# Optimization experiments

Hardware: AMD Instinct MI355X
Metric: run time of the kernel (lower is better)

The kernel has to match this reference:

```python
import jax, jax.numpy as jnp
import numpy as np

T = 256        # number of save/step points
BATCH = 2048   # batched trajectories
DATA = 32      # state dim (data_size)
WIDTH = 128    # MLP width
DELAYS = (1.0, 2.0)  # constant delays tau_j (all >> dt so lookups are in the past)


def setup_inputs() -> dict:
    key = jax.random.key(0)
    ks = jax.random.split(key, 5)
    ts = jnp.linspace(0.0, 10.0, T, dtype=jnp.float32)
    y0 = jax.random.normal(ks[0], (BATCH, DATA), dtype=jnp.float32)
    in_size = (len(DELAYS) + 1) * DATA  # (nb_delays + 1) * data_size

    def lin(k, o, i):
        kw, kb = jax.random.split(k)
        lim = 1.0 / np.sqrt(i)
        W = jax.random.uniform(kw, (o, i), jnp.float32, -lim, lim)
        b = jax.random.uniform(kb, (o,), jnp.float32, -lim, lim)
        return W, b

    W0, b0 = lin(ks[1], WIDTH, in_size)   # in -> width
    W1, b1 = lin(ks[2], WIDTH, WIDTH)     # hidden
    W2, b2 = lin(ks[3], WIDTH, WIDTH)     # hidden
    W3, b3 = lin(ks[4], DATA, WIDTH)      # width -> out (no activation)
    return dict(ts=ts, y0=y0, W0=W0, b0=b0, W1=W1, b1=b1, W2=W2, b2=b2, W3=W3, b3=b3)


def _mlp(x, W0, b0, W1, b1, W2, b2, W3, b3):
    # eqx.nn.MLP(depth=3, activation=relu): 4 linears, relu after hidden layers
    h = jax.nn.relu(x @ W0.T + b0)
    h = jax.nn.relu(h @ W1.T + b1)
    h = jax.nn.relu(h @ W2.T + b2)
    return h @ W3.T + b3


def _solve(ts, y0, params):
    t0 = ts[0]
    dt0 = ts[1] - ts[0]

    def lookup(buf, t):
        # linear interpolation of stored history on the uniform grid;
        # t <= t0 clips to index 0 where buf[0] == y0 (constant initial history)
        s = jnp.clip((t - t0) / dt0, 0.0, T - 1.0)
        i0 = jnp.floor(s).astype(jnp.int32)
        i1 = jnp.minimum(i0 + 1, T - 1)
        w = s - i0.astype(s.dtype)
        return (1.0 - w) * buf[i0] + w * buf[i1]

    def f(t, y, buf):
        hist = [lookup(buf, t - tau) for tau in DELAYS]
        return _mlp(jnp.concatenate([y] + hist, axis=-1), *params)

    buf0 = jnp.zeros((T, BATCH, DATA), y0.dtype).at[0].set(y0)

    def step(carry, inp):
        y, buf = carry
        i, t, t_next = inp
        dt = t_next - t
        # Bosh3 / Bogacki-Shampine stages
        k1 = f(t, y, buf)
        k2 = f(t + 0.5 * dt, y + 0.5 * dt * k1, buf)
        k3 = f(t + 0.75 * dt, y + 0.75 * dt * k2, buf)
        y_next = y + dt * (2.0 / 9.0 * k1 + 1.0 / 3.0 * k2 + 4.0 / 9.0 * k3)
        buf = buf.at[i + 1].set(y_next)
        return (y_next, buf), y_next

    xs = (jnp.arange(T - 1), ts[:-1], ts[1:])
    (_, _), ys_tail = jax.lax.scan(step, (y0, buf0), xs)
    return jnp.concatenate([y0[None], ys_tail], axis=0)  # [T, BATCH, DATA]


def reference(ts, y0, W0, b0, W1, b1, W2, b2, W3, b3):
    ys = _solve(ts, y0, (W0, b0, W1, b1, W2, b2, W3, b3))
    return ys, jnp.int32(T - 1)  # (solution.ys, num_steps)
```

## Files before the change

kernel.cpp:

```cpp
#include <hip/hip_runtime.h>

#define TT 256
#define BATCH 2048
#define DATA 32
#define WSLOTS 52

typedef __bf16 bf16x8 __attribute__((ext_vector_type(8)));
typedef float f32x4 __attribute__((ext_vector_type(4)));

#define MFMA(A, B, C) __builtin_amdgcn_mfma_f32_16x16x32_bf16((A), (B), (C), 0, 0, 0)

union bfp2 { uint2 u; __bf16 b[4]; };
union bfp4 { uint4 q; bf16x8 v; __bf16 b[8]; };

__device__ __forceinline__ bf16x8 ldw8(const float* __restrict__ p) {
    float4 a = *(const float4*)p;
    float4 b = *(const float4*)(p + 4);
    bf16x8 r;
    r[0] = (__bf16)a.x; r[1] = (__bf16)a.y; r[2] = (__bf16)a.z; r[3] = (__bf16)a.w;
    r[4] = (__bf16)b.x; r[5] = (__bf16)b.y; r[6] = (__bf16)b.z; r[7] = (__bf16)b.w;
    return r;
}

__device__ __forceinline__ bf16x8 ldx(const char* base, int row, int kbyte) {
    return *(const bf16x8*)(base + row * 256 + (kbyte ^ ((row & 7) << 4)));
}

#define HID1(WF, KC, SRC, DST, BI)                                                    \
    {                                                                                 \
        bf16x8 xf[4];                                                                 \
        _Pragma("unroll") for (int kc = 0; kc < (KC); ++kc)                           \
            xf[kc] = ldx(SRC, m, kc * 64 + g * 16);                                   \
        f32x4 a0 = BI;                                                                \
        _Pragma("unroll") for (int kc = 0; kc < (KC); ++kc)                           \
            a0 = MFMA(WF[kc], xf[kc], a0);                                            \
        bfp2 p0;                                                                      \
        _Pragma("unroll") for (int j = 0; j < 4; ++j)                                 \
            p0.b[j] = (__bf16)fmaxf(a0[j], 0.0f);                                     \
        *(uint2*)((DST) + m * 256 + ((tbB2 + g * 8) ^ sw)) = p0.u;                    \
    }

#define PRELERP(TQT, XDST)                                                            \
    {                                                                                 \
        const int   dl  = wv - 2;                                                     \
        const float tau = dl ? 2.0f : 1.0f;                                           \
        float s = ((TQT) - tau - t0v) * ivd0;                                         \
        s = fminf(fmaxf(s, 0.0f), 255.0f);                                            \
        const int   i0 = (int)s;                                                      \
        const int   i1 = min(i0 + 1, TT - 1);                                         \
        const float w  = s - (float)i0;                                               \
        bfp4 pa, pb, pr;                                                              \
        pa.v = *(const bf16x8*)(hists + (i0 % WSLOTS) * 1280 + m * 80 + g * 16);      \
        pb.v = *(const bf16x8*)(hists + (i1 % WSLOTS) * 1280 + m * 80 + g * 16);      \
        _Pragma("unroll") for (int e = 0; e < 8; ++e) {                               \
            const float va = (float)pa.b[e];                                          \
            pr.b[e] = (__bf16)fmaf(w, (float)pb.b[e] - va, va);                       \
        }                                                                             \
        *(bf16x8*)((XDST) + dl * 1280 + m * 80 + g * 16) = pr.v;                      \
    }

#define DO_STAGE(USEK, CST, KP, KD, XSRC, XDST, TQT)                                  \
    {                                                                                 \
                                 \
        bfp4 xf0;                                                                     \
        _Pragma("unroll") for (int e = 0; e < 8; ++e)                                 \
            xf0.b[e] = (__bf16)((USEK) ? fmaf((CST) * dt, KP[e], y[e]) : y[e]);       \
        bf16x8 xl1 = *(const bf16x8*)((XSRC) + m * 80 + g * 16);                      \
        bf16x8 xl2 = *(const bf16x8*)((XSRC) + 1280 + m * 80 + g * 16);               \
        f32x4 a0 = bias0;                                                             \
        a0 = MFMA(W0f[0], xf0.v, a0);                                                 \
        a0 = MFMA(W0f[1], xl1, a0);                                                   \
        a0 = MFMA(W0f[2], xl2, a0);                                                   \
        bfp2 p0;                                                                      \
        _Pragma("unroll") for (int j = 0; j < 4; ++j)                                 \
            p0.b[j] = (__bf16)fmaxf(a0[j], 0.0f);                                     \
        *(uint2*)(hA + m * 256 + ((tbB2 + g * 8) ^ sw)) = p0.u;                       \
        __syncthreads();                                                              \
        HID1(W1f, 4, hA, hB, bias1)                                                   \
        __syncthreads();                                                              \
        HID1(W2f, 4, hB, hA, bias2)                                                   \
        __syncthreads();                                                              \
        if (wv < 2) {                      \
            bf16x8 xf[4];                                                             \
            _Pragma("unroll") for (int kc = 0; kc < 4; ++kc)                          \
                xf[kc] = ldx(hA, m, kc * 64 + g * 16);                                \
            f32x4 a = bias3;                                                          \
            _Pragma("unroll") for (int kc = 0; kc < 4; ++kc)                          \
                a = MFMA(W3f[kc], xf[kc], a);                                         \
            *(f32x4*)(kbuf + m * 128 + (((wv * 4 + g) ^ (m & 7)) << 4)) = a;          \
        } else if (wv < 4) {                                                          \
            PRELERP(TQT, XDST)                                                        \
        }                                                                             \
        __syncthreads();                                                              \
        {                           \
            f32x4 q0 = *(const f32x4*)(kbuf + m * 128 + (((2 * g) ^ (m & 7)) << 4));  \
            f32x4 q1 = *(const f32x4*)(kbuf + m * 128 + (((2 * g + 1) ^ (m & 7)) << 4)); \
            _Pragma("unroll") for (int j = 0; j < 4; ++j) {                           \
                KD[j] = q0[j]; KD[4 + j] = q1[j];                                     \
            }                                                                         \
        }                                                                             \
    }

__global__ __launch_bounds__(512, 1) void dde_8w(
    const float* __restrict__ ts, const float* __restrict__ y0,
    const float* __restrict__ W0, const float* __restrict__ b0,
    const float* __restrict__ W1, const float* __restrict__ b1,
    const float* __restrict__ W2, const float* __restrict__ b2,
    const float* __restrict__ W3, const float* __restrict__ b3,
    float* __restrict__ out)
{
    __shared__ __align__(16) char hists[WSLOTS * 1280];
    __shared__ __align__(16) char xb0[2 * 1280];
    __shared__ __align__(16) char xb1[2 * 1280];
    __shared__ __align__(16) char xb2[2 * 1280];
    __shared__ __align__(16) char hA[16 * 256];
    __shared__ __align__(16) char hB[16 * 256];
    __shared__ __align__(16) char kbuf[16 * 128];
    __shared__ float tsb[TT];

    const int tid  = threadIdx.x;
    const int lane = tid & 63;
    const int wv   = tid >> 6;
    const int m    = lane & 15;
    const int g    = lane >> 4;
    const int tbB2 = wv * 32;
    const int sw   = (m & 7) << 4;
    const int R0   = blockIdx.x * 16;

    for (int idx = tid; idx < WSLOTS * 320; idx += 512) ((unsigned*)hists)[idx] = 0u;
    if (tid < TT) tsb[tid] = ts[tid];

    bf16x8 W0f[3], W1f[4], W2f[4], W3f[4];
    {
        const int rw = wv * 16 + m;
        #pragma unroll
        for (int kc = 0; kc < 3; ++kc) W0f[kc] = ldw8(W0 + rw * 96 + kc * 32 + g * 8);
        #pragma unroll
        for (int kc = 0; kc < 4; ++kc) W1f[kc] = ldw8(W1 + rw * 128 + kc * 32 + g * 8);
        #pragma unroll
        for (int kc = 0; kc < 4; ++kc) W2f[kc] = ldw8(W2 + rw * 128 + kc * 32 + g * 8);
        const int rw3 = (wv & 1) * 16 + m;
        #pragma unroll
        for (int kc = 0; kc < 4; ++kc) W3f[kc] = ldw8(W3 + rw3 * 128 + kc * 32 + g * 8);
    }
    f32x4 bias0, bias1, bias2, bias3;
    bias0 = *(const f32x4*)(b0 + wv * 16 + g * 4);
    bias1 = *(const f32x4*)(b1 + wv * 16 + g * 4);
    bias2 = *(const f32x4*)(b2 + wv * 16 + g * 4);
    bias3 = *(const f32x4*)(b3 + (wv & 1) * 16 + g * 4);

    __syncthreads();

    float y[8], k1[8], k2[8], k3[8];
    {
        float4 v0 = *(const float4*)(y0 + (R0 + m) * DATA + g * 8);
        float4 v1 = *(const float4*)(y0 + (R0 + m) * DATA + g * 8 + 4);
        y[0] = v0.x; y[1] = v0.y; y[2] = v0.z; y[3] = v0.w;
        y[4] = v1.x; y[5] = v1.y; y[6] = v1.z; y[7] = v1.w;
        #pragma unroll
        for (int e = 0; e < 8; ++e) { k1[e] = 0.0f; k2[e] = 0.0f; k3[e] = 0.0f; }
        if (wv == 0) {
            bfp4 p;
            #pragma unroll
            for (int e = 0; e < 8; ++e) p.b[e] = (__bf16)y[e];
            *(bf16x8*)(hists + m * 80 + g * 16) = p.v;
            *(float4*)(out + (R0 + m) * DATA + g * 8) = v0;
            *(float4*)(out + (R0 + m) * DATA + g * 8 + 4) = v1;
        }
    }
    if (blockIdx.x == 0 && tid == 0)
        out[(size_t)TT * BATCH * DATA] = 255.0f;
    __syncthreads();

    const float t0v  = tsb[0];
    const float ivd0 = 1.0f / (tsb[1] - tsb[0]);

    if (wv >= 2 && wv < 4) {
        const float dt0 = tsb[1] - tsb[0];
        PRELERP(t0v, xb0)
        PRELERP(fmaf(0.5f, dt0, t0v), xb1)
        PRELERP(fmaf(0.75f, dt0, t0v), xb2)
    }
    __syncthreads();

    #pragma unroll 1
    for (int i = 0; i < TT - 1; ++i) {
        const float t   = tsb[i];
        const float tn  = tsb[i + 1];
        const float dt  = tn - t;
        const float tnn = tsb[min(i + 2, TT - 1)];
        const float dtn = tnn - tn;

        DO_STAGE(0, 0.0f,  k1, k1, xb0, xb2, fmaf(0.75f, dt, t))
        DO_STAGE(1, 0.5f,  k1, k2, xb1, xb0, tn)
        DO_STAGE(2, 0.75f, k2, k3, xb2, xb1, fmaf(0.5f, dtn, tn))

        {
            #pragma unroll
            for (int e = 0; e < 8; ++e) {
                const float ks = (2.0f / 9.0f) * k1[e] + (1.0f / 3.0f) * k2[e]
                               + (4.0f / 9.0f) * k3[e];
                y[e] = fmaf(dt, ks, y[e]);
            }
            if (wv == 0) {
                bfp4 p;
                #pragma unroll
                for (int e = 0; e < 8; ++e) p.b[e] = (__bf16)y[e];
                *(bf16x8*)(hists + ((i + 1) % WSLOTS) * 1280 + m * 80 + g * 16) = p.v;
                float4 o0, o1;
                o0.x = y[0]; o0.y = y[1]; o0.z = y[2]; o0.w = y[3];
                o1.x = y[4]; o1.y = y[5]; o1.z = y[6]; o1.w = y[7];
                float* op = out + (size_t)(i + 1) * BATCH * DATA + (R0 + m) * DATA + g * 8;
                *(float4*)op = o0;
                *(float4*)(op + 4) = o1;
            }
        }
    }
}

extern "C" void kernel_launch(void* const* d_in, const int* in_sizes, int n_in,
                              void* d_out, int out_size, void* d_ws, size_t ws_size,
                              hipStream_t stream) {
    const float* ts = (const float*)d_in[0];
    const float* y0 = (const float*)d_in[1];
    const float* W0 = (const float*)d_in[2];
    const float* b0 = (const float*)d_in[3];
    const float* W1 = (const float*)d_in[4];
    const float* b1 = (const float*)d_in[5];
    const float* W2 = (const float*)d_in[6];
    const float* b2 = (const float*)d_in[7];
    const float* W3 = (const float*)d_in[8];
    const float* b3 = (const float*)d_in[9];

    dde_8w<<<dim3(BATCH / 16), dim3(512), 0, stream>>>(
        ts, y0, W0, b0, W1, b1, W2, b2, W3, b3, (float*)d_out);
}
```

Before: 717.6 us.

## Replicate output layer in every wave to drop a barrier and shared k buffer

```diff
diff --git a/kernel.cpp b/kernel.cpp
--- a/kernel.cpp
+++ b/kernel.cpp
@@ -10,8 +10,9 @@
 
 #define MFMA(A, B, C) __builtin_amdgcn_mfma_f32_16x16x32_bf16((A), (B), (C), 0, 0, 0)
 
-union bfp2 { uint2 u; __bf16 b[4]; };
-union bfp4 { uint4 q; bf16x8 v; __bf16 b[8]; };
+union bfp2 { unsigned u; __bf16 b[2]; };
+union bfq  { uint2 u; __bf16 b[4]; };
+union bfx8 { uint4 q; bf16x8 v; __bf16 b[8]; unsigned w[4]; };
 
 __device__ __forceinline__ bf16x8 ldw8(const float* __restrict__ p) {
     float4 a = *(const float4*)p;
@@ -31,77 +32,112 @@
         bf16x8 xf[4];                                                                 \
         _Pragma("unroll") for (int kc = 0; kc < (KC); ++kc)                           \
             xf[kc] = ldx(SRC, m, kc * 64 + g * 16);                                   \
-        f32x4 a0 = BI;                                                                \
+        f32x4 ac = BI;                                                                \
         _Pragma("unroll") for (int kc = 0; kc < (KC); ++kc)                           \
-            a0 = MFMA(WF[kc], xf[kc], a0);                                            \
-        bfp2 p0;                                                                      \
+            ac = MFMA(WF[kc], xf[kc], ac);                                            \
+        bfq p0;                                                                       \
         _Pragma("unroll") for (int j = 0; j < 4; ++j)                                 \
-            p0.b[j] = (__bf16)fmaxf(a0[j], 0.0f);                                     \
+            p0.b[j] = (__bf16)fmaxf(ac[j], 0.0f);                                     \
         *(uint2*)((DST) + m * 256 + ((tbB2 + g * 8) ^ sw)) = p0.u;                    \
     }
 
-#define PRELERP(TQT, XDST)                                                            \
+#define LERP2(TQT, O1, O2)                                                            \
     {                                                                                 \
-        const int   dl  = wv - 2;                                                     \
-        const float tau = dl ? 2.0f : 1.0f;                                           \
-        float s = ((TQT) - tau - t0v) * ivd0;                                         \
-        s = fminf(fmaxf(s, 0.0f), 255.0f);                                            \
-        const int   i0 = (int)s;                                                      \
-        const int   i1 = min(i0 + 1, TT - 1);                                         \
-        const float w  = s - (float)i0;                                               \
-        bfp4 pa, pb, pr;                                                              \
-        pa.v = *(const bf16x8*)(hists + (i0 % WSLOTS) * 1280 + m * 80 + g * 16);      \
-        pb.v = *(const bf16x8*)(hists + (i1 % WSLOTS) * 1280 + m * 80 + g * 16);      \
-        _Pragma("unroll") for (int e = 0; e < 8; ++e) {                               \
-            const float va = (float)pa.b[e];                                          \
-            pr.b[e] = (__bf16)fmaf(w, (float)pb.b[e] - va, va);                       \
-        }                                                                             \
-        *(bf16x8*)((XDST) + dl * 1280 + m * 80 + g * 16) = pr.v;                      \
-    }
-
-#define DO_STAGE(USEK, CST, KP, KD, XSRC, XDST, TQT)                                  \
+        _Pragma("unroll") for (int dl = 0; dl < 2; ++dl) {                            \
+            const float tau = dl ? 2.0f : 1.0f;                                       \
+            float s = ((TQT) - tau - t0v) * ivd0;                                     \
+            s = fminf(fmaxf(s, 0.0f), 255.0f);                                        \
+            const int   i0 = (int)s;                                                  \
+            const int   i1 = min(i0 + 1, TT - 1);                                     \
+            const float w  = s - (float)i0;                                           \
+            bfx8 pa, pb, pr;                                                          \
+            pa.v = *(const bf16x8*)(hists + (i0 % WSLOTS) * 1280 + m * 80 + g * 16);  \
+            pb.v = *(const bf16x8*)(hists + (i1 % WSLOTS) * 1280 + m * 80 + g * 16);  \
+            _Pragma("unroll") for (int e = 0; e < 8; ++e) {                           \
+                const float va = (float)pa.b[e];                                      \
+                pr.b[e] = (__bf16)fmaf(w, (float)pb.b[e] - va, va);                   \
+            }                                                                         \
+            if (dl == 0) O1 = pr.v; else O2 = pr.v;                                   \
+        }                                                                             \
+    }
+
+#define DO_STAGE(USEK, CST, KP, KD, XI1, XI2, XO1, XO2, TQN, FIN, I)                  \
     {                                                                                 \
-                                 \
-        bfp4 xf0;                                                                     \
-        _Pragma("unroll") for (int e = 0; e < 8; ++e)                                 \
-            xf0.b[e] = (__bf16)((USEK) ? fmaf((CST) * dt, KP[e], y[e]) : y[e]);       \
-        bf16x8 xl1 = *(const bf16x8*)((XSRC) + m * 80 + g * 16);                      \
-        bf16x8 xl2 = *(const bf16x8*)((XSRC) + 1280 + m * 80 + g * 16);               \
-        f32x4 a0 = bias0;                                                             \
-        a0 = MFMA(W0f[0], xf0.v, a0);                                                 \
-        a0 = MFMA(W0f[1], xl1, a0);                                                   \
-        a0 = MFMA(W0f[2], xl2, a0);                                                   \
-        bfp2 p0;                                                                      \
-        _Pragma("unroll") for (int j = 0; j < 4; ++j)                                 \
-            p0.b[j] = (__bf16)fmaxf(a0[j], 0.0f);                                     \
-        *(uint2*)(hA + m * 256 + ((tbB2 + g * 8) ^ sw)) = p0.u;                       \
+                      \
+        float yst[2][4];                                                              \
+        _Pragma("unroll") for (int t2 = 0; t2 < 2; ++t2)                              \
+            _Pragma("unroll") for (int j = 0; j < 4; ++j)                             \
+                yst[t2][j] = (USEK) ? fmaf((CST) * dt, KP[t2][j], y[t2][j])           \
+                                    : y[t2][j];                                       \
+        unsigned pk2[2][2];                                                           \
+        _Pragma("unroll") for (int t2 = 0; t2 < 2; ++t2)                              \
+            _Pragma("unroll") for (int s2 = 0; s2 < 2; ++s2) {                        \
+                bfp2 pp;                                                              \
+                pp.b[0] = (__bf16)yst[t2][2 * s2];                                    \
+                pp.b[1] = (__bf16)yst[t2][2 * s2 + 1];                                \
+                pk2[t2][s2] = pp.u;                                                   \
+            }                                                                         \
+        bfx8 xf0;                                                                     \
+        _Pragma("unroll") for (int s2 = 0; s2 < 2; ++s2) {                            \
+            int aa = __builtin_amdgcn_ds_bpermute(pa0, (int)pk2[0][s2]);              \
+            int bb = __builtin_amdgcn_ds_bpermute(pa0, (int)pk2[1][s2]);              \
+            int cc = __builtin_amdgcn_ds_bpermute(pa1, (int)pk2[0][s2]);              \
+            int dd = __builtin_amdgcn_ds_bpermute(pa1, (int)pk2[1][s2]);              \
+            xf0.w[s2]     = tsel ? (unsigned)bb : (unsigned)aa;                       \
+            xf0.w[2 + s2] = tsel ? (unsigned)dd : (unsigned)cc;                       \
+        }                                                                             \
+        {                                                                             \
+            f32x4 a0c = bias0;                                                        \
+            a0c = MFMA(W0f[1], XI1, a0c);         \
+            a0c = MFMA(W0f[2], XI2, a0c);                                             \
+            a0c = MFMA(W0f[0], xf0.v, a0c);                                           \
+            bfq p0;                                                                   \
+            _Pragma("unroll") for (int j = 0; j < 4; ++j)                             \
+                p0.b[j] = (__bf16)fmaxf(a0c[j], 0.0f);                                \
+            *(uint2*)(hA + m * 256 + ((tbB2 + g * 8) ^ sw)) = p0.u;                   \
+        }                                                                             \
         __syncthreads();                                                              \
         HID1(W1f, 4, hA, hB, bias1)                                                   \
         __syncthreads();                                                              \
-        HID1(W2f, 4, hB, hA, bias2)                                                   \
+        HID1(W2f, 4, hB, hC, bias2)                                                   \
         __syncthreads();                                                              \
-        if (wv < 2) {                      \
-            bf16x8 xf[4];                                                             \
+        {        \
+            LERP2(TQN, XO1, XO2)                                                      \
+            bf16x8 hx[4];                                                             \
             _Pragma("unroll") for (int kc = 0; kc < 4; ++kc)                          \
-                xf[kc] = ldx(hA, m, kc * 64 + g * 16);                                \
-            f32x4 a = bias3;                                                          \
-            _Pragma("unroll") for (int kc = 0; kc < 4; ++kc)                          \
-                a = MFMA(W3f[kc], xf[kc], a);                                         \
-            *(f32x4*)(kbuf + m * 128 + (((wv * 4 + g) ^ (m & 7)) << 4)) = a;          \
-        } else if (wv < 4) {                                                          \
-            PRELERP(TQT, XDST)                                                        \
-        }                                                                             \
-        __syncthreads();                                                              \
-        {                           \
-            f32x4 q0 = *(const f32x4*)(kbuf + m * 128 + (((2 * g) ^ (m & 7)) << 4));  \
-            f32x4 q1 = *(const f32x4*)(kbuf + m * 128 + (((2 * g + 1) ^ (m & 7)) << 4)); \
-            _Pragma("unroll") for (int j = 0; j < 4; ++j) {                           \
-                KD[j] = q0[j]; KD[4 + j] = q1[j];                                     \
-            }                                                                         \
-        }                                                                             \
-    }
-
-__global__ __launch_bounds__(512, 1) void dde_8w(
+                hx[kc] = ldx(hC, m, kc * 64 + g * 16);                                \
+            _Pragma("unroll") for (int t2 = 0; t2 < 2; ++t2) {                        \
+                f32x4 a3 = bias3D[t2];                                                \
+                _Pragma("unroll") for (int kc = 0; kc < 4; ++kc)                      \
+                    a3 = MFMA(W3f[t2][kc], hx[kc], a3);                               \
+                KD[t2] = a3;                                                          \
+            }                                                                         \
+            if (FIN) {                 \
+                _Pragma("unroll") for (int t2 = 0; t2 < 2; ++t2)                      \
+                    _Pragma("unroll") for (int j = 0; j < 4; ++j) {                   \
+                        const float ks = (2.0f / 9.0f) * k1[t2][j]                    \
+                                       + (1.0f / 3.0f) * k2[t2][j]                    \
+                                       + (4.0f / 9.0f) * KD[t2][j];                   \
+                        y[t2][j] = fmaf(dt, ks, y[t2][j]);                            \
+                    }                                                                 \
+                if (wv == 0) {                                                        \
+                    _Pragma("unroll") for (int t2 = 0; t2 < 2; ++t2) {                \
+                        bfq p; float4 v;                                              \
+                        p.b[0] = (__bf16)y[t2][0]; p.b[1] = (__bf16)y[t2][1];         \
+                        p.b[2] = (__bf16)y[t2][2]; p.b[3] = (__bf16)y[t2][3];         \
+                        v.x = y[t2][0]; v.y = y[t2][1];                               \
+                        v.z = y[t2][2]; v.w = y[t2][3];                               \
+                        *(uint2*)(hists + (((I) + 1) % WSLOTS) * 1280 + m * 80        \
+                                  + t2 * 32 + g * 8) = p.u;                           \
+                        *(float4*)(out + (size_t)((I) + 1) * BATCH * DATA             \
+                                   + (R0 + m) * DATA + t2 * 16 + g * 4) = v;          \
+                    }                                                                 \
+                }                                                                     \
+            }                                                                         \
+        }                                                                             \
+    }
+
+__global__ __launch_bounds__(512, 1) void dde_p(
     const float* __restrict__ ts, const float* __restrict__ y0,
     const float* __restrict__ W0, const float* __restrict__ b0,
     const float* __restrict__ W1, const float* __restrict__ b1,
@@ -110,12 +146,9 @@
     float* __restrict__ out)
 {
     __shared__ __align__(16) char hists[WSLOTS * 1280];
-    __shared__ __align__(16) char xb0[2 * 1280];
-    __shared__ __align__(16) char xb1[2 * 1280];
-    __shared__ __align__(16) char xb2[2 * 1280];
     __shared__ __align__(16) char hA[16 * 256];
     __shared__ __align__(16) char hB[16 * 256];
-    __shared__ __align__(16) char kbuf[16 * 128];
+    __shared__ __align__(16) char hC[16 * 256];
     __shared__ float tsb[TT];
 
     const int tid  = threadIdx.x;
@@ -126,11 +159,14 @@
     const int tbB2 = wv * 32;
     const int sw   = (m & 7) << 4;
     const int R0   = blockIdx.x * 16;
+    const int pa0  = (m + ((g & 1) << 5)) << 2;
+    const int pa1  = pa0 + 64;
+    const int tsel = g >> 1;
 
     for (int idx = tid; idx < WSLOTS * 320; idx += 512) ((unsigned*)hists)[idx] = 0u;
     if (tid < TT) tsb[tid] = ts[tid];
 
-    bf16x8 W0f[3], W1f[4], W2f[4], W3f[4];
+    bf16x8 W0f[3], W1f[4], W2f[4], W3f[2][4];
     {
         const int rw = wv * 16 + m;
         #pragma unroll
@@ -139,33 +175,34 @@
         for (int kc = 0; kc < 4; ++kc) W1f[kc] = ldw8(W1 + rw * 128 + kc * 32 + g * 8);
         #pragma unroll
         for (int kc = 0; kc < 4; ++kc) W2f[kc] = ldw8(W2 + rw * 128 + kc * 32 + g * 8);
-        const int rw3 = (wv & 1) * 16 + m;
-        #pragma unroll
-        for (int kc = 0; kc < 4; ++kc) W3f[kc] = ldw8(W3 + rw3 * 128 + kc * 32 + g * 8);
-    }
-    f32x4 bias0, bias1, bias2, bias3;
+        #pragma unroll
+        for (int t2 = 0; t2 < 2; ++t2)
+            #pragma unroll
+            for (int kc = 0; kc < 4; ++kc)
+                W3f[t2][kc] = ldw8(W3 + (t2 * 16 + m) * 128 + kc * 32 + g * 8);
+    }
+    f32x4 bias0, bias1, bias2, bias3D[2];
     bias0 = *(const f32x4*)(b0 + wv * 16 + g * 4);
     bias1 = *(const f32x4*)(b1 + wv * 16 + g * 4);
     bias2 = *(const f32x4*)(b2 + wv * 16 + g * 4);
-    bias3 = *(const f32x4*)(b3 + (wv & 1) * 16 + g * 4);
+    #pragma unroll
+    for (int t2 = 0; t2 < 2; ++t2)
+        bias3D[t2] = *(const f32x4*)(b3 + t2 * 16 + g * 4);
 
     __syncthreads();
 
-    float y[8], k1[8], k2[8], k3[8];
-    {
-        float4 v0 = *(const float4*)(y0 + (R0 + m) * DATA + g * 8);
-        float4 v1 = *(const float4*)(y0 + (R0 + m) * DATA + g * 8 + 4);
-        y[0] = v0.x; y[1] = v0.y; y[2] = v0.z; y[3] = v0.w;
-        y[4] = v1.x; y[5] = v1.y; y[6] = v1.z; y[7] = v1.w;
-        #pragma unroll
-        for (int e = 0; e < 8; ++e) { k1[e] = 0.0f; k2[e] = 0.0f; k3[e] = 0.0f; }
+    f32x4 y[2], k1[2], k2[2], k3[2];
+    #pragma unroll
+    for (int t2 = 0; t2 < 2; ++t2) {
+        float4 vv = *(const float4*)(y0 + (R0 + m) * DATA + t2 * 16 + g * 4);
+        y[t2][0] = vv.x; y[t2][1] = vv.y; y[t2][2] = vv.z; y[t2][3] = vv.w;
+        k1[t2] = f32x4{0.f, 0.f, 0.f, 0.f}; k2[t2] = k1[t2]; k3[t2] = k1[t2];
         if (wv == 0) {
-            bfp4 p;
-            #pragma unroll
-            for (int e = 0; e < 8; ++e) p.b[e] = (__bf16)y[e];
-            *(bf16x8*)(hists + m * 80 + g * 16) = p.v;
-            *(float4*)(out + (R0 + m) * DATA + g * 8) = v0;
-            *(float4*)(out + (R0 + m) * DATA + g * 8 + 4) = v1;
+            bfq p;
+            p.b[0] = (__bf16)vv.x; p.b[1] = (__bf16)vv.y;
+            p.b[2] = (__bf16)vv.z; p.b[3] = (__bf16)vv.w;
+            *(uint2*)(hists + m * 80 + t2 * 32 + g * 8) = p.u;
+            *(float4*)(out + (R0 + m) * DATA + t2 * 16 + g * 4) = vv;
         }
     }
     if (blockIdx.x == 0 && tid == 0)
@@ -175,46 +212,19 @@
     const float t0v  = tsb[0];
     const float ivd0 = 1.0f / (tsb[1] - tsb[0]);
 
-    if (wv >= 2 && wv < 4) {
-        const float dt0 = tsb[1] - tsb[0];
-        PRELERP(t0v, xb0)
-        PRELERP(fmaf(0.5f, dt0, t0v), xb1)
-        PRELERP(fmaf(0.75f, dt0, t0v), xb2)
-    }
-    __syncthreads();
+    bf16x8 xlA1, xlA2, xlB1, xlB2, xlC1, xlC2;
+    LERP2(t0v, xlA1, xlA2)
 
     #pragma unroll 1
     for (int i = 0; i < TT - 1; ++i) {
-        const float t   = tsb[i];
-        const float tn  = tsb[i + 1];
-        const float dt  = tn - t;
-        const float tnn = tsb[min(i + 2, TT - 1)];
-        const float dtn = tnn - tn;
-
-        DO_STAGE(0, 0.0f,  k1, k1, xb0, xb2, fmaf(0.75f, dt, t))
-        DO_STAGE(1, 0.5f,  k1, k2, xb1, xb0, tn)
-        DO_STAGE(2, 0.75f, k2, k3, xb2, xb1, fmaf(0.5f, dtn, tn))
-
-        {
-            #pragma unroll
-            for (int e = 0; e < 8; ++e) {
-                const float ks = (2.0f / 9.0f) * k1[e] + (1.0f / 3.0f) * k2[e]
-                               + (4.0f / 9.0f) * k3[e];
-                y[e] = fmaf(dt, ks, y[e]);
-            }
-            if (wv == 0) {
-                bfp4 p;
-                #pragma unroll
-                for (int e = 0; e < 8; ++e) p.b[e] = (__bf16)y[e];
-                *(bf16x8*)(hists + ((i + 1) % WSLOTS) * 1280 + m * 80 + g * 16) = p.v;
-                float4 o0, o1;
-                o0.x = y[0]; o0.y = y[1]; o0.z = y[2]; o0.w = y[3];
-                o1.x = y[4]; o1.y = y[5]; o1.z = y[6]; o1.w = y[7];
-                float* op = out + (size_t)(i + 1) * BATCH * DATA + (R0 + m) * DATA + g * 8;
-                *(float4*)op = o0;
-                *(float4*)(op + 4) = o1;
-            }
-        }
+        const float t  = tsb[i];
+        const float tn = tsb[i + 1];
+        const float dt = tn - t;
+
+        DO_STAGE(0, 0.0f,  k1, k1, xlA1, xlA2, xlB1, xlB2, fmaf(0.5f, dt, t), 0, i)
+        DO_STAGE(1, 0.5f,  k1, k2, xlB1, xlB2, xlC1, xlC2, fmaf(0.75f, dt, t), 0, i)
+        DO_STAGE(2, 0.75f, k2, k3, xlC1, xlC2, xlA1, xlA2, tn, 1, i)
+
     }
 }
 
@@ -232,6 +242,6 @@
     const float* W3 = (const float*)d_in[8];
     const float* b3 = (const float*)d_in[9];
 
-    dde_8w<<<dim3(BATCH / 16), dim3(512), 0, stream>>>(
+    dde_p<<<dim3(BATCH / 16), dim3(512), 0, stream>>>(
         ts, y0, W0, b0, W1, b1, W2, b2, W3, b3, (float*)d_out);
 }
```

Result: slower. 933.1 us (+30.0%).

## Fold output layer into first layer via precomputed W0y·W3 product

Applied to the files above, without the earlier changes.

```diff
diff --git a/kernel.cpp b/kernel.cpp
--- a/kernel.cpp
+++ b/kernel.cpp
@@ -26,82 +26,93 @@
     return *(const bf16x8*)(base + row * 256 + (kbyte ^ ((row & 7) << 4)));
 }
 
-#define HID1(WF, KC, SRC, DST, BI)                                                    \
+#define LERP2(TQT, O1, O2)                                                            \
+    {                                                                                 \
+        _Pragma("unroll") for (int dl = 0; dl < 2; ++dl) {                            \
+            const float tau = dl ? 2.0f : 1.0f;                                       \
+            float s = ((TQT) - tau - t0v) * ivd0;                                     \
+            s = fminf(fmaxf(s, 0.0f), 255.0f);                                        \
+            const int   i0 = (int)s;                                                  \
+            const int   i1 = min(i0 + 1, TT - 1);                                     \
+            const float w  = s - (float)i0;                                           \
+            bfp4 pa, pb, pr;                                                          \
+            pa.v = *(const bf16x8*)(hists + (i0 % WSLOTS) * 1280 + m * 80 + g * 16);  \
+            pb.v = *(const bf16x8*)(hists + (i1 % WSLOTS) * 1280 + m * 80 + g * 16);  \
+            _Pragma("unroll") for (int e = 0; e < 8; ++e) {                           \
+                const float va = (float)pa.b[e];                                      \
+                pr.b[e] = (__bf16)fmaf(w, (float)pb.b[e] - va, va);                   \
+            }                                                                         \
+            if (dl == 0) O1 = pr.v; else O2 = pr.v;                                   \
+        }                                                                             \
+    }
+
+#define SEGB()                                                                        \
     {                                                                                 \
         bf16x8 xf[4];                                                                 \
-        _Pragma("unroll") for (int kc = 0; kc < (KC); ++kc)                           \
-            xf[kc] = ldx(SRC, m, kc * 64 + g * 16);                                   \
-        f32x4 a0 = BI;                                                                \
-        _Pragma("unroll") for (int kc = 0; kc < (KC); ++kc)                           \
-            a0 = MFMA(WF[kc], xf[kc], a0);                                            \
+        _Pragma("unroll") for (int kc = 0; kc < 4; ++kc)                              \
+            xf[kc] = ldx(hA, m, kc * 64 + g * 16);                                    \
+        f32x4 a0 = b1D, cc = {0.f, 0.f, 0.f, 0.f};                                    \
+        __builtin_amdgcn_s_setprio(1);                                                \
+        a0 = MFMA(W1f[0], xf[0], a0); cc = MFMA(W1f[2], xf[2], cc);                   \
+        a0 = MFMA(W1f[1], xf[1], a0); cc = MFMA(W1f[3], xf[3], cc);                   \
+        __builtin_amdgcn_s_setprio(0);                                                \
         bfp2 p0;                                                                      \
         _Pragma("unroll") for (int j = 0; j < 4; ++j)                                 \
-            p0.b[j] = (__bf16)fmaxf(a0[j], 0.0f);                                     \
-        *(uint2*)((DST) + m * 256 + ((tbB2 + g * 8) ^ sw)) = p0.u;                    \
-    }
-
-#define PRELERP(TQT, XDST)                                                            \
+            p0.b[j] = (__bf16)fmaxf(a0[j] + cc[j], 0.0f);                             \
+        *(uint2*)(hB + m * 256 + ((tbB2 + g * 8) ^ sw)) = p0.u;                       \
+    }
+
+#define SEGC(COEF, FIRST, STOREH2, DSTBUF)                                            \
     {                                                                                 \
-        const int   dl  = wv - 2;                                                     \
-        const float tau = dl ? 2.0f : 1.0f;                                           \
-        float s = ((TQT) - tau - t0v) * ivd0;                                         \
-        s = fminf(fmaxf(s, 0.0f), 255.0f);                                            \
-        const int   i0 = (int)s;                                                      \
-        const int   i1 = min(i0 + 1, TT - 1);                                         \
-        const float w  = s - (float)i0;                                               \
-        bfp4 pa, pb, pr;                                                              \
-        pa.v = *(const bf16x8*)(hists + (i0 % WSLOTS) * 1280 + m * 80 + g * 16);      \
-        pb.v = *(const bf16x8*)(hists + (i1 % WSLOTS) * 1280 + m * 80 + g * 16);      \
-        _Pragma("unroll") for (int e = 0; e < 8; ++e) {                               \
-            const float va = (float)pa.b[e];                                          \
-            pr.b[e] = (__bf16)fmaf(w, (float)pb.b[e] - va, va);                       \
-        }                                                                             \
-        *(bf16x8*)((XDST) + dl * 1280 + m * 80 + g * 16) = pr.v;                      \
-    }
-
-#define DO_STAGE(USEK, CST, KP, KD, XSRC, XDST, TQT)                                  \
+        bf16x8 xf[4];                                                                 \
+        _Pragma("unroll") for (int kc = 0; kc < 4; ++kc)                              \
+            xf[kc] = ldx(hB, m, kc * 64 + g * 16);                                    \
+        f32x4 a0 = b2D, cc = {0.f, 0.f, 0.f, 0.f};                                    \
+        __builtin_amdgcn_s_setprio(1);                                                \
+        a0 = MFMA(W2f[0], xf[0], a0); cc = MFMA(W2f[2], xf[2], cc);                   \
+        a0 = MFMA(W2f[1], xf[1], a0); cc = MFMA(W2f[3], xf[3], cc);                   \
+        __builtin_amdgcn_s_setprio(0);                                                \
+        f32x4 r;                                                                      \
+        _Pragma("unroll") for (int j = 0; j < 4; ++j)                                 \
+            r[j] = fmaxf(a0[j] + cc[j], 0.0f);                                        \
+        if (FIRST) { _Pragma("unroll") for (int j = 0; j < 4; ++j)                    \
+                         hsreg[j] = (COEF) * r[j]; }                                  \
+        else       { _Pragma("unroll") for (int j = 0; j < 4; ++j)                    \
+                         hsreg[j] = fmaf((COEF), r[j], hsreg[j]); }                   \
+        bfp2 ph;                                                                      \
+        if (STOREH2) { _Pragma("unroll") for (int j = 0; j < 4; ++j)                  \
+                           ph.b[j] = (__bf16)r[j]; }                                  \
+        else         { _Pragma("unroll") for (int j = 0; j < 4; ++j)                  \
+                           ph.b[j] = (__bf16)hsreg[j]; }                              \
+        *(uint2*)((DSTBUF) + m * 256 + ((tbB2 + g * 8) ^ sw)) = ph.u;                 \
+    }
+
+#define SEGA23(HIN, CST)                                                              \
     {                                                                                 \
-                                 \
-        bfp4 xf0;                                                                     \
-        _Pragma("unroll") for (int e = 0; e < 8; ++e)                                 \
-            xf0.b[e] = (__bf16)((USEK) ? fmaf((CST) * dt, KP[e], y[e]) : y[e]);       \
-        bf16x8 xl1 = *(const bf16x8*)((XSRC) + m * 80 + g * 16);                      \
-        bf16x8 xl2 = *(const bf16x8*)((XSRC) + 1280 + m * 80 + g * 16);               \
-        f32x4 a0 = bias0;                                                             \
-        a0 = MFMA(W0f[0], xf0.v, a0);                                                 \
-        a0 = MFMA(W0f[1], xl1, a0);                                                   \
-        a0 = MFMA(W0f[2], xl2, a0);                                                   \
+        bf16x8 hf[4];                                                                 \
+        _Pragma("unroll") for (int kc = 0; kc < 4; ++kc)                              \
+            hf[kc] = ldx(HIN, m, kc * 64 + g * 16);                                   \
+        f32x4 ta = {0.f, 0.f, 0.f, 0.f}, tc = ta;                                     \
+        __builtin_amdgcn_s_setprio(1);                                                \
+        ta = MFMA(Mf[0], hf[0], ta); tc = MFMA(Mf[2], hf[2], tc);                     \
+        ta = MFMA(Mf[1], hf[1], ta); tc = MFMA(Mf[3], hf[3], tc);                     \
+        __builtin_amdgcn_s_setprio(0);                                                \
+        bf16x8 xl1, xl2;                                                              \
+        LERP2(fmaf(CST, dt, t), xl1, xl2)                                             \
+        f32x4 la = b0D;                                                               \
+        __builtin_amdgcn_s_setprio(1);                                                \
+        la = MFMA(W0lf[0], xl1, la);                                                  \
+        la = MFMA(W0lf[1], xl2, la);                                                  \
+        __builtin_amdgcn_s_setprio(0);                                                \
+        const float cdt = (CST) * dt;                                                 \
         bfp2 p0;                                                                      \
         _Pragma("unroll") for (int j = 0; j < 4; ++j)                                 \
-            p0.b[j] = (__bf16)fmaxf(a0[j], 0.0f);                                     \
+            p0.b[j] = (__bf16)fmaxf(fmaf(cdt, ta[j] + tc[j] + c0v[j], u[j]) + la[j],  \
+                                    0.0f);                                            \
         *(uint2*)(hA + m * 256 + ((tbB2 + g * 8) ^ sw)) = p0.u;                       \
-        __syncthreads();                                                              \
-        HID1(W1f, 4, hA, hB, bias1)                                                   \
-        __syncthreads();                                                              \
-        HID1(W2f, 4, hB, hA, bias2)                                                   \
-        __syncthreads();                                                              \
-        if (wv < 2) {                      \
-            bf16x8 xf[4];                                                             \
-            _Pragma("unroll") for (int kc = 0; kc < 4; ++kc)                          \
-                xf[kc] = ldx(hA, m, kc * 64 + g * 16);                                \
-            f32x4 a = bias3;                                                          \
-            _Pragma("unroll") for (int kc = 0; kc < 4; ++kc)                          \
-                a = MFMA(W3f[kc], xf[kc], a);                                         \
-            *(f32x4*)(kbuf + m * 128 + (((wv * 4 + g) ^ (m & 7)) << 4)) = a;          \
-        } else if (wv < 4) {                                                          \
-            PRELERP(TQT, XDST)                                                        \
-        }                                                                             \
-        __syncthreads();                                                              \
-        {                           \
-            f32x4 q0 = *(const f32x4*)(kbuf + m * 128 + (((2 * g) ^ (m & 7)) << 4));  \
-            f32x4 q1 = *(const f32x4*)(kbuf + m * 128 + (((2 * g + 1) ^ (m & 7)) << 4)); \
-            _Pragma("unroll") for (int j = 0; j < 4; ++j) {                           \
-                KD[j] = q0[j]; KD[4 + j] = q1[j];                                     \
-            }                                                                         \
-        }                                                                             \
-    }
-
-__global__ __launch_bounds__(512, 1) void dde_8w(
+    }
+
+__global__ __launch_bounds__(512, 1) void dde_fu(
     const float* __restrict__ ts, const float* __restrict__ y0,
     const float* __restrict__ W0, const float* __restrict__ b0,
     const float* __restrict__ W1, const float* __restrict__ b1,
@@ -110,12 +121,12 @@
     float* __restrict__ out)
 {
     __shared__ __align__(16) char hists[WSLOTS * 1280];
-    __shared__ __align__(16) char xb0[2 * 1280];
-    __shared__ __align__(16) char xb1[2 * 1280];
-    __shared__ __align__(16) char xb2[2 * 1280];
     __shared__ __align__(16) char hA[16 * 256];
     __shared__ __align__(16) char hB[16 * 256];
-    __shared__ __align__(16) char kbuf[16 * 128];
+    __shared__ __align__(16) char h2a[16 * 256];
+    __shared__ __align__(16) char h2b[16 * 256];
+    __shared__ __align__(16) char hsb[16 * 256];
+    __shared__ __align__(16) float ybuf[512];
     __shared__ float tsb[TT];
 
     const int tid  = threadIdx.x;
@@ -130,11 +141,11 @@
     for (int idx = tid; idx < WSLOTS * 320; idx += 512) ((unsigned*)hists)[idx] = 0u;
     if (tid < TT) tsb[tid] = ts[tid];
 
-    bf16x8 W0f[3], W1f[4], W2f[4], W3f[4];
+    bf16x8 W0lf[2], W1f[4], W2f[4], W3f[4], Mf[4];
     {
         const int rw = wv * 16 + m;
         #pragma unroll
-        for (int kc = 0; kc < 3; ++kc) W0f[kc] = ldw8(W0 + rw * 96 + kc * 32 + g * 8);
+        for (int kc = 0; kc < 2; ++kc) W0lf[kc] = ldw8(W0 + rw * 96 + 32 + kc * 32 + g * 8);
         #pragma unroll
         for (int kc = 0; kc < 4; ++kc) W1f[kc] = ldw8(W1 + rw * 128 + kc * 32 + g * 8);
         #pragma unroll
@@ -143,30 +154,62 @@
         #pragma unroll
         for (int kc = 0; kc < 4; ++kc) W3f[kc] = ldw8(W3 + rw3 * 128 + kc * 32 + g * 8);
     }
-    f32x4 bias0, bias1, bias2, bias3;
-    bias0 = *(const f32x4*)(b0 + wv * 16 + g * 4);
-    bias1 = *(const f32x4*)(b1 + wv * 16 + g * 4);
-    bias2 = *(const f32x4*)(b2 + wv * 16 + g * 4);
-    bias3 = *(const f32x4*)(b3 + (wv & 1) * 16 + g * 4);
+    {
+        float w0y[32];
+        const float* w0r = W0 + (wv * 16 + m) * 96;
+        #pragma unroll
+        for (int d = 0; d < 32; ++d) w0y[d] = w0r[d];
+        #pragma unroll
+        for (int kc = 0; kc < 4; ++kc) {
+            bf16x8 f;
+            #pragma unroll
+            for (int e = 0; e < 8; ++e) {
+                const int h = kc * 32 + g * 8 + e;
+                float acc = 0.f;
+                #pragma unroll
+                for (int d = 0; d < 32; ++d) acc = fmaf(w0y[d], W3[d * 128 + h], acc);
+                f[e] = (__bf16)acc;
+            }
+            Mf[kc] = f;
+        }
+    }
+    f32x4 b0D = *(const f32x4*)(b0 + wv * 16 + g * 4);
+    f32x4 b1D = *(const f32x4*)(b1 + wv * 16 + g * 4);
+    f32x4 b2D = *(const f32x4*)(b2 + wv * 16 + g * 4);
+    f32x4 b3D = *(const f32x4*)(b3 + (wv & 1) * 16 + g * 4);
+    f32x4 c0v, u;
+    {
+        const float* yr = y0 + (R0 + m) * DATA;
+        #pragma unroll
+        for (int j = 0; j < 4; ++j) {
+            const float* w0r = W0 + (wv * 16 + g * 4 + j) * 96;
+            float a = 0.f, uu = 0.f;
+            #pragma unroll
+            for (int d = 0; d < 32; ++d) {
+                a  = fmaf(w0r[d], b3[d], a);
+                uu = fmaf(w0r[d], yr[d], uu);
+            }
+            c0v[j] = a; u[j] = uu;
+        }
+    }
+    f32x4 y;
+    #pragma unroll
+    for (int j = 0; j < 4; ++j)
+        y[j] = y0[(R0 + m) * DATA + (wv & 1) * 16 + g * 4 + j];
 
     __syncthreads();
 
-    float y[8], k1[8], k2[8], k3[8];
-    {
+    if (wv == 0) {
         float4 v0 = *(const float4*)(y0 + (R0 + m) * DATA + g * 8);
         float4 v1 = *(const float4*)(y0 + (R0 + m) * DATA + g * 8 + 4);
-        y[0] = v0.x; y[1] = v0.y; y[2] = v0.z; y[3] = v0.w;
-        y[4] = v1.x; y[5] = v1.y; y[6] = v1.z; y[7] = v1.w;
-        #pragma unroll
-        for (int e = 0; e < 8; ++e) { k1[e] = 0.0f; k2[e] = 0.0f; k3[e] = 0.0f; }
-        if (wv == 0) {
-            bfp4 p;
-            #pragma unroll
-            for (int e = 0; e < 8; ++e) p.b[e] = (__bf16)y[e];
-            *(bf16x8*)(hists + m * 80 + g * 16) = p.v;
-            *(float4*)(out + (R0 + m) * DATA + g * 8) = v0;
-            *(float4*)(out + (R0 + m) * DATA + g * 8 + 4) = v1;
-        }
+        bfp4 p;
+        p.b[0] = (__bf16)v0.x; p.b[1] = (__bf16)v0.y;
+        p.b[2] = (__bf16)v0.z; p.b[3] = (__bf16)v0.w;
+        p.b[4] = (__bf16)v1.x; p.b[5] = (__bf16)v1.y;
+        p.b[6] = (__bf16)v1.z; p.b[7] = (__bf16)v1.w;
+        *(bf16x8*)(hists + m * 80 + g * 16) = p.v;
+        *(float4*)(out + (R0 + m) * DATA + g * 8) = v0;
+        *(float4*)(out + (R0 + m) * DATA + g * 8 + 4) = v1;
     }
     if (blockIdx.x == 0 && tid == 0)
         out[(size_t)TT * BATCH * DATA] = 255.0f;
@@ -175,46 +218,99 @@
     const float t0v  = tsb[0];
     const float ivd0 = 1.0f / (tsb[1] - tsb[0]);
 
-    if (wv >= 2 && wv < 4) {
-        const float dt0 = tsb[1] - tsb[0];
-        PRELERP(t0v, xb0)
-        PRELERP(fmaf(0.5f, dt0, t0v), xb1)
-        PRELERP(fmaf(0.75f, dt0, t0v), xb2)
-    }
-    __syncthreads();
-
     #pragma unroll 1
     for (int i = 0; i < TT - 1; ++i) {
-        const float t   = tsb[i];
-        const float tn  = tsb[i + 1];
-        const float dt  = tn - t;
-        const float tnn = tsb[min(i + 2, TT - 1)];
-        const float dtn = tnn - tn;
-
-        DO_STAGE(0, 0.0f,  k1, k1, xb0, xb2, fmaf(0.75f, dt, t))
-        DO_STAGE(1, 0.5f,  k1, k2, xb1, xb0, tn)
-        DO_STAGE(2, 0.75f, k2, k3, xb2, xb1, fmaf(0.5f, dtn, tn))
+        const float t  = tsb[i];
+        const float dt = tsb[i + 1] - t;
+        f32x4 hsreg;
 
         {
+            if (i > 0) {
+                const float dtp = t - tsb[i - 1];
+                bf16x8 hs[4];
+                #pragma unroll
+                for (int kc = 0; kc < 4; ++kc) hs[kc] = ldx(hsb, m, kc * 64 + g * 16);
+                f32x4 ta = {0.f, 0.f, 0.f, 0.f}, tc = ta;
+                __builtin_amdgcn_s_setprio(1);
+                ta = MFMA(Mf[0], hs[0], ta); tc = MFMA(Mf[2], hs[2], tc);
+                ta = MFMA(Mf[1], hs[1], ta); tc = MFMA(Mf[3], hs[3], tc);
+                __builtin_amdgcn_s_setprio(0);
+                #pragma unroll
+                for (int j = 0; j < 4; ++j)
+                    u[j] = fmaf(dtp, ta[j] + tc[j] + c0v[j], u[j]);
+                if (wv < 2) {
+                    f32x4 ya = {0.f, 0.f, 0.f, 0.f}, yc = ya;
+                    __builtin_amdgcn_s_setprio(1);
+                    ya = MFMA(W3f[0], hs[0], ya); yc = MFMA(W3f[2], hs[2], yc);
+                    ya = MFMA(W3f[1], hs[1], ya); yc = MFMA(W3f[3], hs[3], yc);
+                    __builtin_amdgcn_s_setprio(0);
+                    #pragma unroll
+                    for (int j = 0; j < 4; ++j) {
+                        y[j] = fmaf(dtp, ya[j] + yc[j] + b3D[j], y[j]);
+                        *(__bf16*)(hists + (i % WSLOTS) * 1280 + m * 80
+                                   + wv * 32 + g * 8 + 2 * j) = (__bf16)y[j];
+                        ybuf[m * 32 + wv * 16 + g * 4 + j] = y[j];
+                    }
+                }
+            }
+            bf16x8 xl1, xl2;
+            LERP2(t, xl1, xl2)
+            f32x4 la = b0D;
+            __builtin_amdgcn_s_setprio(1);
+            la = MFMA(W0lf[0], xl1, la);
+            la = MFMA(W0lf[1], xl2, la);
+            __builtin_amdgcn_s_setprio(0);
+            bfp2 p0;
             #pragma unroll
-            for (int e = 0; e < 8; ++e) {
-                const float ks = (2.0f / 9.0f) * k1[e] + (1.0f / 3.0f) * k2[e]
-                               + (4.0f / 9.0f) * k3[e];
-                y[e] = fmaf(dt, ks, y[e]);
-            }
-            if (wv == 0) {
-                bfp4 p;
-                #pragma unroll
-                for (int e = 0; e < 8; ++e) p.b[e] = (__bf16)y[e];
-                *(bf16x8*)(hists + ((i + 1) % WSLOTS) * 1280 + m * 80 + g * 16) = p.v;
-                float4 o0, o1;
-                o0.x = y[0]; o0.y = y[1]; o0.z = y[2]; o0.w = y[3];
-                o1.x = y[4]; o1.y = y[5]; o1.z = y[6]; o1.w = y[7];
-                float* op = out + (size_t)(i + 1) * BATCH * DATA + (R0 + m) * DATA + g * 8;
-                *(float4*)op = o0;
-                *(float4*)(op + 4) = o1;
-            }
-        }
+            for (int j = 0; j < 4; ++j)
+                p0.b[j] = (__bf16)fmaxf(u[j] + la[j], 0.0f);
+            *(uint2*)(hA + m * 256 + ((tbB2 + g * 8) ^ sw)) = p0.u;
+        }
+        __syncthreads();
+        SEGB()
+        __syncthreads();
+        SEGC(2.0f / 9.0f, 1, 1, h2a)
+        if (i > 0 && wv < 2) {
+            const int L = wv * 64 + lane;
+            float4 yv = *(const float4*)(ybuf + L * 4);
+            *(float4*)(out + (size_t)i * BATCH * DATA
+                       + (R0 + (L >> 3)) * DATA + (L & 7) * 4) = yv;
+        }
+        __syncthreads();
+        SEGA23(h2a, 0.5f)
+        __syncthreads();
+        SEGB()
+        __syncthreads();
+        SEGC(1.0f / 3.0f, 0, 1, h2b)
+        __syncthreads();
+        SEGA23(h2b, 0.75f)
+        __syncthreads();
+        SEGB()
+        __syncthreads();
+        SEGC(4.0f / 9.0f, 0, 0, hsb)
+        __syncthreads();
+    }
+
+    if (wv < 2) {
+        const float dtp = tsb[TT - 1] - tsb[TT - 2];
+        bf16x8 hs[4];
+        #pragma unroll
+        for (int kc = 0; kc < 4; ++kc) hs[kc] = ldx(hsb, m, kc * 64 + g * 16);
+        f32x4 ya = {0.f, 0.f, 0.f, 0.f}, yc = ya;
+        ya = MFMA(W3f[0], hs[0], ya); yc = MFMA(W3f[2], hs[2], yc);
+        ya = MFMA(W3f[1], hs[1], ya); yc = MFMA(W3f[3], hs[3], yc);
+        #pragma unroll
+        for (int j = 0; j < 4; ++j) {
+            y[j] = fmaf(dtp, ya[j] + yc[j] + b3D[j], y[j]);
+            ybuf[m * 32 + (wv & 1) * 16 + g * 4 + j] = y[j];
+        }
+    }
+    __syncthreads();
+    if (wv < 2) {
+        const int L = wv * 64 + lane;
+        float4 yv = *(const float4*)(ybuf + L * 4);
+        *(float4*)(out + (size_t)(TT - 1) * BATCH * DATA
+                   + (R0 + (L >> 3)) * DATA + (L & 7) * 4) = yv;
     }
 }
 
@@ -232,6 +328,6 @@
     const float* W3 = (const float*)d_in[8];
     const float* b3 = (const float*)d_in[9];
 
-    dde_8w<<<dim3(BATCH / 16), dim3(512), 0, stream>>>(
+    dde_fu<<<dim3(BATCH / 16), dim3(512), 0, stream>>>(
         ts, y0, W0, b0, W1, b1, W2, b2, W3, b3, (float*)d_out);
 }
```

After: 842.0 us. 17.3% more time.
